# Kernel optimization log

Measured on AMD Instinct MI355X. Metric: run time of the kernel, lower is better.

## Reference

```python
import jax, jax.numpy as jnp
import numpy as np

B, TQ, TKV, D, H = 4, 1024, 2048, 1024, 16
DH = D // H


def setup_inputs() -> dict:
    key = jax.random.key(0)
    ks = jax.random.split(key, 12)
    s = 0.02
    return {
        "x": jax.random.normal(ks[0], (B, TQ, D), jnp.float32),
        "k_cache": jax.random.normal(ks[1], (B, TKV, D), jnp.float32),
        "v_cache": jax.random.normal(ks[2], (B, TKV, D), jnp.float32),
        "mask": jnp.zeros((TQ, TKV), jnp.float32),  # additive attention bias
        "Wq": jax.random.normal(ks[3], (D, D), jnp.float32) * s,
        "bq": jax.random.normal(ks[4], (D,), jnp.float32) * s,
        "Wk": jax.random.normal(ks[5], (D, D), jnp.float32) * s,  # key: no bias (Whisper-style)
        "Wv": jax.random.normal(ks[6], (D, D), jnp.float32) * s,
        "bv": jax.random.normal(ks[7], (D,), jnp.float32) * s,
        "Wo": jax.random.normal(ks[8], (D, D), jnp.float32) * s,
        "bo": jax.random.normal(ks[9], (D,), jnp.float32) * s,
    }


def reference(x, k_cache, v_cache, mask, Wq, bq, Wk, Wv, bv, Wo, bo):
    b, tq, d = x.shape
    scale = (d // H) ** -0.25
    # QKV projections (torch Linear: y = x @ W.T + b)
    q = x @ Wq.T + bq                      # [B,Tq,D]
    k_new = x @ Wk.T                       # [B,Tq,D] (key has no bias)
    v_new = x @ Wv.T + bv                  # [B,Tq,D]
    # KV-cache append: write last Tq positions
    k_cache = k_cache.at[:, -tq:, :].set(k_new)
    v_cache = v_cache.at[:, -tq:, :].set(v_new)
    # split heads
    qh = q.reshape(b, tq, H, DH) * scale           # [B,Tq,H,Dh]
    kh = k_cache.reshape(b, -1, H, DH) * scale     # [B,Tkv,H,Dh]
    vh = v_cache.reshape(b, -1, H, DH)             # [B,Tkv,H,Dh]
    qk = jnp.einsum("bqhd,bkhd->bhqk", qh, kh) + mask  # [B,H,Tq,Tkv]
    w = jax.nn.softmax(qk.astype(jnp.float32), axis=-1).astype(qh.dtype)
    wv = jnp.einsum("bhqk,bkhd->bqhd", w, vh).reshape(b, tq, d)
    out = wv @ Wo.T + bo
    return out, k_cache, v_cache
```

## Files before the change

### kernel.cpp

```cpp
#include <hip/hip_runtime.h>
#include <hip/hip_bf16.h>


typedef __bf16 bf16_t;
typedef __attribute__((ext_vector_type(4))) float f32x4;
typedef __attribute__((ext_vector_type(8))) __bf16 bf16x8;
typedef __attribute__((ext_vector_type(4))) __bf16 bf16x4;
typedef __attribute__((ext_vector_type(4))) unsigned short u16x4;

__device__ inline bf16x4 cvt4(float4 f) {
    bf16x4 o;
    o.x = (bf16_t)f.x; o.y = (bf16_t)f.y; o.z = (bf16_t)f.z; o.w = (bf16_t)f.w;
    return o;
}

__device__ inline void gload_lds16(const void* g, void* s) {
    __builtin_amdgcn_global_load_lds(
        (const __attribute__((address_space(1))) void*)g,
        (__attribute__((address_space(3))) void*)s, 16, 0, 0);
}

__device__ inline unsigned cvt_pk_bf16(float lo, float hi) {
    unsigned r;
    asm("v_cvt_pk_bf16_f32 %0, %1, %2" : "=v"(r) : "v"(lo), "v"(hi));
    return r;
}
__device__ inline void pswap32(unsigned& a, unsigned& b) {
    asm("v_permlane32_swap_b32 %0, %1" : "+v"(a), "+v"(b));
}
__device__ inline void pswap16(unsigned& a, unsigned& b) {
    asm("v_permlane16_swap_b32 %0, %1" : "+v"(a), "+v"(b));
}

#if __has_builtin(__builtin_amdgcn_exp2f)
__device__ inline float exp2_fast(float x) { return __builtin_amdgcn_exp2f(x); }
#else
__device__ inline float exp2_fast(float x) { return exp2f(x); }
#endif


__global__ void cast_f32_bf16_k(const float* __restrict__ src, bf16_t* __restrict__ dst, int n4) {
    int i = blockIdx.x * blockDim.x + threadIdx.x;
    if (i >= n4) return;
    float4 f = reinterpret_cast<const float4*>(src)[i];
    reinterpret_cast<bf16x4*>(dst)[i] = cvt4(f);
}

__global__ void build_wqkv_k(const float* __restrict__ Wq, const float* __restrict__ Wk,
                             const float* __restrict__ Wv, bf16_t* __restrict__ dst) {
    int i = blockIdx.x * blockDim.x + threadIdx.x;
    if (i >= 786432) return;
    int e0 = i * 4;
    int row = e0 >> 10;
    const float* src;
    if (row < 1024)       src = Wq + e0;
    else if (row < 2048)  src = Wk + (e0 - 1048576);
    else                  src = Wv + (e0 - 2097152);
    float4 f = *reinterpret_cast<const float4*>(src);
    reinterpret_cast<bf16x4*>(dst)[i] = cvt4(f);
}

__global__ void build_bias_k(const float* __restrict__ bq, const float* __restrict__ bv,
                             float* __restrict__ bias) {
    int i = blockIdx.x * blockDim.x + threadIdx.x;
    if (i >= 3072) return;
    float v;
    if (i < 1024)      v = bq[i];
    else if (i < 2048) v = 0.f;
    else               v = bv[i - 2048];
    bias[i] = v;
}

__global__ void copy_old2_k(const float* __restrict__ kc, const float* __restrict__ vc,
                            float* __restrict__ kout, float* __restrict__ vout,
                            bf16_t* __restrict__ k_bf) {
    int i = blockIdx.x * blockDim.x + threadIdx.x;
    if (i >= 2097152) return;
    int which = i >> 20;
    int ii = i & 1048575;
    int b = ii >> 18;
    int r = ii & 262143;
    size_t off = (size_t)b * 2097152 + (size_t)r * 4;
    if (which == 0) {
        float4 f = *reinterpret_cast<const float4*>(kc + off);
        *reinterpret_cast<float4*>(kout + off) = f;
        reinterpret_cast<bf16x4*>(k_bf + off)[0] = cvt4(f);
    } else {
        float4 f = *reinterpret_cast<const float4*>(vc + off);
        *reinterpret_cast<float4*>(vout + off) = f;
    }
}

__global__ __launch_bounds__(256) void transpose_v_k(const float* __restrict__ vout,
                                                     bf16_t* __restrict__ vT) {
    __shared__ bf16_t t[64][65];
    int blk = blockIdx.x;
    int kvt = blk >> 6;
    int bh  = blk & 63;
    int b = bh >> 4, h = bh & 15;
    int kv0 = kvt * 64;
    int tid = threadIdx.x;
    int c = tid & 63, r0 = tid >> 6;
    #pragma unroll
    for (int rr = r0; rr < 64; rr += 4)
        t[rr][c] = (bf16_t)vout[((size_t)b * 2048 + kv0 + rr) * 1024 + h * 64 + c];
    __syncthreads();
    #pragma unroll
    for (int dd = r0; dd < 64; dd += 4)
        vT[((size_t)bh * 64 + dd) * 2048 + kv0 + c] = t[c][dd];
}

__global__ void mask_bf16_k(const float* __restrict__ mask, bf16_t* __restrict__ maskB) {
    int i = blockIdx.x * blockDim.x + threadIdx.x;
    if (i >= 2097152) return;
    int r   = i & 3;
    int c16 = (i >> 2) & 15;
    int qd  = (i >> 6) & 3;
    int kb  = (i >> 8) & 127;
    int qb  = i >> 15;
    float v = mask[(size_t)(qb * 16 + c16) * 2048 + kb * 16 + qd * 4 + r] * 1.4426950408889634f;
    maskB[i] = (bf16_t)v;
}

#define LDF(bufp, row, off) (*reinterpret_cast<const bf16x8*>(&(bufp)[(row) * 64 + (off)]))

__global__ __launch_bounds__(512, 2) void gemm8_k(const bf16_t* __restrict__ A,
                                                  const bf16_t* __restrict__ Bw,
                                                  const float* __restrict__ bias,
                                                  bf16_t* __restrict__ q_bf,
                                                  float* __restrict__ kout,
                                                  bf16_t* __restrict__ k_bf,
                                                  float* __restrict__ vout) {
    const int K = 1024;
    __shared__ __align__(16) bf16_t As[2][16384];
    __shared__ __align__(16) bf16_t Bs[2][16384];
    int m0 = blockIdx.x * 256, n0 = blockIdx.y * 256;
    int tid = threadIdx.x;
    int lane = tid & 63, w = tid >> 6;
    int wrM = w >> 2, wrN = w & 3;
    int col16 = lane & 15, quad = lane >> 4;
    int cx = (quad ^ (col16 & 7)) * 8;

    int sr = tid >> 3;
    int scb = ((tid & 7) ^ (sr & 7)) * 8;
    const bf16_t* ga = A + (size_t)(m0 + sr) * K + scb;
    const bf16_t* gb = Bw + (size_t)(n0 + sr) * K + scb;
    int ldst = sr * 64 + (tid & 7) * 8;

    auto stageA = [&](int d, int kt) {
        size_t ko = (size_t)kt * 64;
        gload_lds16(ga + ko, &As[d][ldst]);
        gload_lds16(ga + 64 * (size_t)K + ko, &As[d][ldst + 4096]);
        gload_lds16(ga + 128 * (size_t)K + ko, &As[d][ldst + 8192]);
        gload_lds16(ga + 192 * (size_t)K + ko, &As[d][ldst + 12288]);
    };
    auto stageB = [&](int d, int kt) {
        size_t ko = (size_t)kt * 64;
        gload_lds16(gb + ko, &Bs[d][ldst]);
        gload_lds16(gb + 64 * (size_t)K + ko, &Bs[d][ldst + 4096]);
        gload_lds16(gb + 128 * (size_t)K + ko, &Bs[d][ldst + 8192]);
        gload_lds16(gb + 192 * (size_t)K + ko, &Bs[d][ldst + 12288]);
    };

    int arow = wrM * 128 + col16;
    int brow = wrN * 64 + col16;

    f32x4 zero = {0.f, 0.f, 0.f, 0.f};
    f32x4 acc[8][4];
    #pragma unroll
    for (int mi = 0; mi < 8; mi++)
        #pragma unroll
        for (int ni = 0; ni < 4; ni++) acc[mi][ni] = zero;

    stageA(0, 0);
    stageB(0, 0);
    stageA(1, 1);
    asm volatile("s_waitcnt vmcnt(4)" ::: "memory");
    __builtin_amdgcn_s_barrier();

    for (int kt = 0; kt < 16; kt++) {
        int d = kt & 1;
        const bf16_t* Ad = As[d];
        const bf16_t* Bd = Bs[d];
        bf16x8 a0[4][2], bb0[2][2];
        #pragma unroll
        for (int mi = 0; mi < 4; mi++) {
            a0[mi][0] = LDF(Ad, arow + mi * 16, cx);
            a0[mi][1] = LDF(Ad, arow + mi * 16, cx ^ 32);
        }
        #pragma unroll
        for (int ni = 0; ni < 2; ni++) {
            bb0[ni][0] = LDF(Bd, brow + ni * 16, cx);
            bb0[ni][1] = LDF(Bd, brow + ni * 16, cx ^ 32);
        }
        if (kt < 15) stageB(d ^ 1, kt + 1);
        __builtin_amdgcn_s_barrier();
        __builtin_amdgcn_s_setprio(1);
        #pragma unroll
        for (int mi = 0; mi < 4; mi++)
            #pragma unroll
            for (int ni = 0; ni < 2; ni++) {
                acc[mi][ni] = __builtin_amdgcn_mfma_f32_16x16x32_bf16(a0[mi][0], bb0[ni][0], acc[mi][ni], 0, 0, 0);
                acc[mi][ni] = __builtin_amdgcn_mfma_f32_16x16x32_bf16(a0[mi][1], bb0[ni][1], acc[mi][ni], 0, 0, 0);
            }
        __builtin_amdgcn_s_setprio(0);
        __builtin_amdgcn_s_barrier();
        bf16x8 bb1[2][2];
        #pragma unroll
        for (int ni = 0; ni < 2; ni++) {
            bb1[ni][0] = LDF(Bd, brow + 32 + ni * 16, cx);
            bb1[ni][1] = LDF(Bd, brow + 32 + ni * 16, cx ^ 32);
        }
        __builtin_amdgcn_s_barrier();
        __builtin_amdgcn_s_setprio(1);
        #pragma unroll
        for (int mi = 0; mi < 4; mi++)
            #pragma unroll
            for (int ni = 0; ni < 2; ni++) {
                acc[mi][ni + 2] = __builtin_amdgcn_mfma_f32_16x16x32_bf16(a0[mi][0], bb1[ni][0], acc[mi][ni + 2], 0, 0, 0);
                acc[mi][ni + 2] = __builtin_amdgcn_mfma_f32_16x16x32_bf16(a0[mi][1], bb1[ni][1], acc[mi][ni + 2], 0, 0, 0);
            }
        __builtin_amdgcn_s_setprio(0);
        __builtin_amdgcn_s_barrier();
        bf16x8 a1[4][2];
        #pragma unroll
        for (int mi = 0; mi < 4; mi++) {
            a1[mi][0] = LDF(Ad, arow + 64 + mi * 16, cx);
            a1[mi][1] = LDF(Ad, arow + 64 + mi * 16, cx ^ 32);
        }
        __builtin_amdgcn_s_barrier();
        __builtin_amdgcn_s_setprio(1);
        #pragma unroll
        for (int mi = 0; mi < 4; mi++)
            #pragma unroll
            for (int ni = 0; ni < 2; ni++) {
                acc[mi + 4][ni] = __builtin_amdgcn_mfma_f32_16x16x32_bf16(a1[mi][0], bb0[ni][0], acc[mi + 4][ni], 0, 0, 0);
                acc[mi + 4][ni] = __builtin_amdgcn_mfma_f32_16x16x32_bf16(a1[mi][1], bb0[ni][1], acc[mi + 4][ni], 0, 0, 0);
            }
        __builtin_amdgcn_s_setprio(0);
        __builtin_amdgcn_s_barrier();
        if (kt < 14) {
            stageA(d, kt + 2);
            asm volatile("s_waitcnt vmcnt(4)" ::: "memory");
        } else {
            asm volatile("s_waitcnt vmcnt(0)" ::: "memory");
        }
        __builtin_amdgcn_s_barrier();
        __builtin_amdgcn_s_setprio(1);
        #pragma unroll
        for (int mi = 0; mi < 4; mi++)
            #pragma unroll
            for (int ni = 0; ni < 2; ni++) {
                acc[mi + 4][ni + 2] = __builtin_amdgcn_mfma_f32_16x16x32_bf16(a1[mi][0], bb1[ni][0], acc[mi + 4][ni + 2], 0, 0, 0);
                acc[mi + 4][ni + 2] = __builtin_amdgcn_mfma_f32_16x16x32_bf16(a1[mi][1], bb1[ni][1], acc[mi + 4][ni + 2], 0, 0, 0);
            }
        __builtin_amdgcn_s_setprio(0);
        __builtin_amdgcn_s_barrier();
    }

    int mb = m0 + wrM * 128 + quad * 4;
    int nb = n0 + wrN * 64 + col16;
    if (n0 < 1024) {
        #pragma unroll
        for (int ni = 0; ni < 4; ni++) {
            int gn = nb + ni * 16;
            float bia = bias[gn];
            #pragma unroll
            for (int mi = 0; mi < 8; mi++) {
                int gm = mb + mi * 16;
                #pragma unroll
                for (int r = 0; r < 4; r++)
                    q_bf[(size_t)(gm + r) * 1024 + gn] = (bf16_t)(acc[mi][ni][r] + bia);
            }
        }
    } else if (n0 < 2048) {
        #pragma unroll
        for (int ni = 0; ni < 4; ni++) {
            int gn = nb + ni * 16;
            float bia = bias[gn];
            int n2 = gn - 1024;
            #pragma unroll
            for (int mi = 0; mi < 8; mi++) {
                int gm = mb + mi * 16;
                #pragma unroll
                for (int r = 0; r < 4; r++) {
                    int gmr = gm + r;
                    int b = gmr >> 10, t = gmr & 1023;
                    size_t off = ((size_t)b * 2048 + 1024 + t) * 1024 + n2;
                    float v = acc[mi][ni][r] + bia;
                    kout[off] = v;
                    k_bf[off] = (bf16_t)v;
                }
            }
        }
    } else {
        #pragma unroll
        for (int ni = 0; ni < 4; ni++) {
            int gn = nb + ni * 16;
            float bia = bias[gn];
            int n2 = gn - 2048;
            #pragma unroll
            for (int mi = 0; mi < 8; mi++) {
                int gm = mb + mi * 16;
                #pragma unroll
                for (int r = 0; r < 4; r++) {
                    int gmr = gm + r;
                    int b = gmr >> 10, t = gmr & 1023;
                    vout[((size_t)b * 2048 + 1024 + t) * 1024 + n2] = acc[mi][ni][r] + bia;
                }
            }
        }
    }
}

__global__ __launch_bounds__(256) void gemm_wo_k(const bf16_t* __restrict__ A,
                                                 const bf16_t* __restrict__ Bw,
                                                 const float* __restrict__ bias,
                                                 float* __restrict__ out0) {
    const int K = 1024;
    __shared__ __align__(16) bf16_t As[2][4096];
    __shared__ __align__(16) bf16_t Bs[2][4096];
    int m0 = blockIdx.x * 128, n0 = blockIdx.y * 128;
    int tid = threadIdx.x;
    int lane = tid & 63, w = tid >> 6;
    int wr = w >> 1, wc = w & 1;
    int col16 = lane & 15, quad = lane >> 4;

    int srow = tid >> 2;
    int scol = ((tid & 3) ^ ((srow >> 1) & 3)) * 8;
    const bf16_t* ga = A + (size_t)(m0 + srow) * K + scol;
    const bf16_t* gb = Bw + (size_t)(n0 + srow) * K + scol;

    int qsw = (quad ^ ((col16 >> 1) & 3)) * 8;

    f32x4 zero = {0.f, 0.f, 0.f, 0.f};
    f32x4 acc[4][4];
    #pragma unroll
    for (int mi = 0; mi < 4; mi++)
        #pragma unroll
        for (int ni = 0; ni < 4; ni++) acc[mi][ni] = zero;

    auto stageg = [&](int d, int k) {
        gload_lds16(ga + k, &As[d][tid * 8]);
        gload_lds16(ga + (size_t)64 * K + k, &As[d][tid * 8 + 2048]);
        gload_lds16(gb + k, &Bs[d][tid * 8]);
        gload_lds16(gb + (size_t)64 * K + k, &Bs[d][tid * 8 + 2048]);
    };

    stageg(0, 0);
    __syncthreads();
    for (int kb = 0; kb < 32; kb++) {
        int cur = kb & 1;
        if (kb < 31) stageg(cur ^ 1, (kb + 1) * 32);
        bf16x8 af[4], bfr[4];
        #pragma unroll
        for (int mi = 0; mi < 4; mi++)
            af[mi] = *reinterpret_cast<const bf16x8*>(
                &As[cur][(wr * 64 + mi * 16 + col16) * 32 + qsw]);
        #pragma unroll
        for (int ni = 0; ni < 4; ni++)
            bfr[ni] = *reinterpret_cast<const bf16x8*>(
                &Bs[cur][(wc * 64 + ni * 16 + col16) * 32 + qsw]);
        #pragma unroll
        for (int mi = 0; mi < 4; mi++)
            #pragma unroll
            for (int ni = 0; ni < 4; ni++)
                acc[mi][ni] = __builtin_amdgcn_mfma_f32_16x16x32_bf16(
                    af[mi], bfr[ni], acc[mi][ni], 0, 0, 0);
        __syncthreads();
    }

    int mbase = m0 + wr * 64 + quad * 4;
    int nbase = n0 + wc * 64 + col16;
    #pragma unroll
    for (int ni = 0; ni < 4; ni++) {
        int gn = nbase + ni * 16;
        float bia = bias[gn];
        #pragma unroll
        for (int mi = 0; mi < 4; mi++) {
            int gm = mbase + mi * 16;
            #pragma unroll
            for (int r = 0; r < 4; r++)
                out0[(size_t)(gm + r) * 1024 + gn] = acc[mi][ni][r] + bia;
        }
    }
}

__global__ __launch_bounds__(512, 4) void attn_k(const bf16_t* __restrict__ qbf,
                                                 const bf16_t* __restrict__ kbf,
                                                 const bf16_t* __restrict__ vT,
                                                 const bf16_t* __restrict__ maskB,
                                                 bf16_t* __restrict__ wv) {
    __shared__ __align__(16) bf16_t Ks[2][4096];
    __shared__ __align__(16) bf16_t Vs[2][4096];
    int logical = (blockIdx.x & 7) * 64 + (blockIdx.x >> 3);
    int bh = logical >> 3;
    int qtb = logical & 7;
    int b = bh >> 4, h = bh & 15;
    int tid = threadIdx.x, w = tid >> 6, lane = tid & 63;
    int col16 = lane & 15, quad = lane >> 4;
    int c7 = col16 & 7;
    int cx = (quad ^ c7) * 8;
    int qr0 = qtb * 128 + w * 16;

    int sr = tid >> 3, sc = (tid & 7) ^ ((tid >> 3) & 7);
    const bf16_t* kg = kbf + ((size_t)b * 2048 + sr) * 1024 + h * 64 + sc * 8;
    const bf16_t* vg = vT + ((size_t)bh * 64 + sr) * 2048 + sc * 8;
    auto stage = [&](int d, int kv0) {
        gload_lds16(kg + (size_t)kv0 * 1024, &Ks[d][tid * 8]);
        gload_lds16(vg + kv0, &Vs[d][tid * 8]);
    };

    const bf16_t* qrow = qbf + ((size_t)b * 1024 + qr0 + col16) * 1024 + h * 64;
    bf16x8 aq0 = *reinterpret_cast<const bf16x8*>(qrow + quad * 8);
    bf16x8 aq1 = *reinterpret_cast<const bf16x8*>(qrow + 32 + quad * 8);

    const bf16_t* mbase = maskB + (size_t)(qtb * 8 + w) * 32768 + quad * 64 + col16 * 4;

    f32x4 zero = {0.f, 0.f, 0.f, 0.f};
    f32x4 oacc[4];
    #pragma unroll
    for (int dt = 0; dt < 4; dt++) oacc[dt] = zero;
    float lrow = 0.f;

    stage(0, 0);
    __syncthreads();

    for (int t = 0; t < 32; t++) {
        int cur = t & 1;
        if (t < 31) stage(cur ^ 1, (t + 1) * 64);
        unsigned pk[4][2];
        #pragma unroll
        for (int nt = 0; nt < 4; nt++) {
            const bf16_t* kr = &Ks[cur][(nt * 16 + col16) * 64];
            bf16x8 k0 = *reinterpret_cast<const bf16x8*>(kr + cx);
            bf16x8 k1 = *reinterpret_cast<const bf16x8*>(kr + (cx ^ 32));
            f32x4 s = __builtin_amdgcn_mfma_f32_16x16x32_bf16(k0, aq0, zero, 0, 0, 0);
            s = __builtin_amdgcn_mfma_f32_16x16x32_bf16(k1, aq1, s, 0, 0, 0);
            u16x4 m4 = *reinterpret_cast<const u16x4*>(mbase + (size_t)(t * 4 + nt) * 256);
            float p[4];
            #pragma unroll
            for (int r = 0; r < 4; r++) {
                float mv = __builtin_bit_cast(float, (unsigned)m4[r] << 16);
                p[r] = exp2_fast(fmaf(s[r], 0.18033688011112042f, mv));
                lrow += p[r];
            }
            pk[nt][0] = cvt_pk_bf16(p[0], p[1]);
            pk[nt][1] = cvt_pk_bf16(p[2], p[3]);
        }
        union PB { unsigned u[4]; bf16x8 v; };
        PB pf0, pf1;
        {
            unsigned a0 = pk[0][0], b0 = pk[1][0];
            pswap32(a0, b0); pswap16(a0, b0);
            pf0.u[0] = a0; pf0.u[2] = b0;
            unsigned a1 = pk[0][1], b1 = pk[1][1];
            pswap32(a1, b1); pswap16(a1, b1);
            pf0.u[1] = a1; pf0.u[3] = b1;
            unsigned a2 = pk[2][0], b2 = pk[3][0];
            pswap32(a2, b2); pswap16(a2, b2);
            pf1.u[0] = a2; pf1.u[2] = b2;
            unsigned a3 = pk[2][1], b3 = pk[3][1];
            pswap32(a3, b3); pswap16(a3, b3);
            pf1.u[1] = a3; pf1.u[3] = b3;
        }
        #pragma unroll
        for (int dt = 0; dt < 4; dt++) {
            const bf16_t* vr = &Vs[cur][(dt * 16 + col16) * 64];
            bf16x8 v0 = *reinterpret_cast<const bf16x8*>(vr + cx);
            bf16x8 v1 = *reinterpret_cast<const bf16x8*>(vr + (cx ^ 32));
            oacc[dt] = __builtin_amdgcn_mfma_f32_16x16x32_bf16(v0, pf0.v, oacc[dt], 0, 0, 0);
            oacc[dt] = __builtin_amdgcn_mfma_f32_16x16x32_bf16(v1, pf1.v, oacc[dt], 0, 0, 0);
        }
        __syncthreads();
    }

    lrow += __shfl_xor(lrow, 16);
    lrow += __shfl_xor(lrow, 32);
    float inv = 1.f / lrow;
    bf16_t* orow = wv + ((size_t)b * 1024 + qr0 + col16) * 1024 + h * 64 + quad * 4;
    #pragma unroll
    for (int dt = 0; dt < 4; dt++) {
        bf16x4 o4;
        #pragma unroll
        for (int r = 0; r < 4; r++) o4[r] = (bf16_t)(oacc[dt][r] * inv);
        *reinterpret_cast<bf16x4*>(orow + dt * 16) = o4;
    }
}


extern "C" void kernel_launch(void* const* d_in, const int* in_sizes, int n_in,
                              void* d_out, int out_size, void* d_ws, size_t ws_size,
                              hipStream_t stream) {
    const float* x    = (const float*)d_in[0];
    const float* kc   = (const float*)d_in[1];
    const float* vc   = (const float*)d_in[2];
    const float* mask = (const float*)d_in[3];
    const float* Wq   = (const float*)d_in[4];
    const float* bq   = (const float*)d_in[5];
    const float* Wk   = (const float*)d_in[6];
    const float* Wv   = (const float*)d_in[7];
    const float* bv   = (const float*)d_in[8];
    const float* Wo   = (const float*)d_in[9];
    const float* bo   = (const float*)d_in[10];

    float* out0 = (float*)d_out;
    float* kout = out0 + 4194304;
    float* vout = out0 + 12582912;

    char* ws = (char*)d_ws;
    bf16_t* x_bf     = (bf16_t*)(ws);
    bf16_t* wqkv_bf  = (bf16_t*)(ws + 8388608);
    bf16_t* wo_bf    = (bf16_t*)(ws + 14680064);
    float*  bias_qkv = (float*)(ws + 16777216);
    bf16_t* q_bf     = (bf16_t*)(ws + 16789504);
    bf16_t* k_bf     = (bf16_t*)(ws + 25178112);
    bf16_t* vT_bf    = (bf16_t*)(ws + 41955328);
    bf16_t* wv_bf    = (bf16_t*)(ws + 58732544);
    bf16_t* maskB    = (bf16_t*)(ws + 67108864);

    cast_f32_bf16_k<<<4096, 256, 0, stream>>>(x, x_bf, 1048576);
    build_wqkv_k<<<3072, 256, 0, stream>>>(Wq, Wk, Wv, wqkv_bf);
    cast_f32_bf16_k<<<1024, 256, 0, stream>>>(Wo, wo_bf, 262144);
    build_bias_k<<<12, 256, 0, stream>>>(bq, bv, bias_qkv);
    mask_bf16_k<<<8192, 256, 0, stream>>>(mask, maskB);
    copy_old2_k<<<8192, 256, 0, stream>>>(kc, vc, kout, vout, k_bf);
    gemm8_k<<<dim3(16, 12), 512, 0, stream>>>(x_bf, wqkv_bf, bias_qkv,
                                              q_bf, kout, k_bf, vout);
    transpose_v_k<<<2048, 256, 0, stream>>>(vout, vT_bf);
    attn_k<<<512, 512, 0, stream>>>(q_bf, k_bf, vT_bf, maskB, wv_bf);
    gemm_wo_k<<<dim3(32, 8), 256, 0, stream>>>(wv_bf, wo_bf, bo, out0);
}
```

Measured before the change: 316.2 us.

## Use inline-asm LDS reads with explicit waits and remap GEMM block order

Replaces compiler-generated LDS vector loads with inline ds_read_b128 plus explicit lgkmcnt(0) waits and sched barriers in the QKV GEMM, output GEMM and attention kernels. This pins the load/MFMA ordering the code expects. It also permutes the QKV GEMM block index so neighbouring blocks share operand tiles in cache. The attention kernel now waits per tile for its loads, which may serialise LDS latency that the compiler previously hid.

```diff
diff --git a/kernel.cpp b/kernel.cpp
--- a/kernel.cpp
+++ b/kernel.cpp
@@ -19,6 +19,17 @@
         (const __attribute__((address_space(1))) void*)g,
         (__attribute__((address_space(3))) void*)s, 16, 0, 0);
 }
+
+__device__ inline bf16x8 ldsr128(const bf16_t* p) {
+    bf16x8 d;
+    unsigned a = (unsigned)(size_t)(const __attribute__((address_space(3))) bf16_t*)p;
+    asm volatile("ds_read_b128 %0, %1" : "=v"(d) : "v"(a));
+    return d;
+}
+
+#define WAIT_LGKM0 do { asm volatile("s_waitcnt lgkmcnt(0)" ::: "memory"); \
+                        __builtin_amdgcn_sched_barrier(0); } while (0)
+#define WAIT_VM(n) asm volatile("s_waitcnt vmcnt(" #n ")" ::: "memory")
 
 __device__ inline unsigned cvt_pk_bf16(float lo, float hi) {
     unsigned r;
@@ -122,8 +133,6 @@
     maskB[i] = (bf16_t)v;
 }
 
-#define LDF(bufp, row, off) (*reinterpret_cast<const bf16x8*>(&(bufp)[(row) * 64 + (off)]))
-
 __global__ __launch_bounds__(512, 2) void gemm8_k(const bf16_t* __restrict__ A,
                                                   const bf16_t* __restrict__ Bw,
                                                   const float* __restrict__ bias,
@@ -134,7 +143,9 @@
     const int K = 1024;
     __shared__ __align__(16) bf16_t As[2][16384];
     __shared__ __align__(16) bf16_t Bs[2][16384];
-    int m0 = blockIdx.x * 256, n0 = blockIdx.y * 256;
+    int flat = blockIdx.y * 16 + blockIdx.x;
+    int logi = (flat & 7) * 24 + (flat >> 3);
+    int m0 = (logi / 12) * 256, n0 = (logi % 12) * 256;
     int tid = threadIdx.x;
     int lane = tid & 63, w = tid >> 6;
     int wrM = w >> 2, wrN = w & 3;
@@ -175,7 +186,7 @@
     stageA(0, 0);
     stageB(0, 0);
     stageA(1, 1);
-    asm volatile("s_waitcnt vmcnt(4)" ::: "memory");
+    WAIT_VM(4);
     __builtin_amdgcn_s_barrier();
 
     for (int kt = 0; kt < 16; kt++) {
@@ -185,16 +196,19 @@
         bf16x8 a0[4][2], bb0[2][2];
         #pragma unroll
         for (int mi = 0; mi < 4; mi++) {
-            a0[mi][0] = LDF(Ad, arow + mi * 16, cx);
-            a0[mi][1] = LDF(Ad, arow + mi * 16, cx ^ 32);
+            const bf16_t* p = &Ad[(arow + mi * 16) * 64];
+            a0[mi][0] = ldsr128(p + cx);
+            a0[mi][1] = ldsr128(p + (cx ^ 32));
         }
         #pragma unroll
         for (int ni = 0; ni < 2; ni++) {
-            bb0[ni][0] = LDF(Bd, brow + ni * 16, cx);
-            bb0[ni][1] = LDF(Bd, brow + ni * 16, cx ^ 32);
+            const bf16_t* p = &Bd[(brow + ni * 16) * 64];
+            bb0[ni][0] = ldsr128(p + cx);
+            bb0[ni][1] = ldsr128(p + (cx ^ 32));
         }
         if (kt < 15) stageB(d ^ 1, kt + 1);
         __builtin_amdgcn_s_barrier();
+        WAIT_LGKM0;
         __builtin_amdgcn_s_setprio(1);
         #pragma unroll
         for (int mi = 0; mi < 4; mi++)
@@ -208,10 +222,12 @@
         bf16x8 bb1[2][2];
         #pragma unroll
         for (int ni = 0; ni < 2; ni++) {
-            bb1[ni][0] = LDF(Bd, brow + 32 + ni * 16, cx);
-            bb1[ni][1] = LDF(Bd, brow + 32 + ni * 16, cx ^ 32);
-        }
-        __builtin_amdgcn_s_barrier();
+            const bf16_t* p = &Bd[(brow + 32 + ni * 16) * 64];
+            bb1[ni][0] = ldsr128(p + cx);
+            bb1[ni][1] = ldsr128(p + (cx ^ 32));
+        }
+        __builtin_amdgcn_s_barrier();
+        WAIT_LGKM0;
         __builtin_amdgcn_s_setprio(1);
         #pragma unroll
         for (int mi = 0; mi < 4; mi++)
@@ -225,10 +241,12 @@
         bf16x8 a1[4][2];
         #pragma unroll
         for (int mi = 0; mi < 4; mi++) {
-            a1[mi][0] = LDF(Ad, arow + 64 + mi * 16, cx);
-            a1[mi][1] = LDF(Ad, arow + 64 + mi * 16, cx ^ 32);
-        }
-        __builtin_amdgcn_s_barrier();
+            const bf16_t* p = &Ad[(arow + 64 + mi * 16) * 64];
+            a1[mi][0] = ldsr128(p + cx);
+            a1[mi][1] = ldsr128(p + (cx ^ 32));
+        }
+        __builtin_amdgcn_s_barrier();
+        WAIT_LGKM0;
         __builtin_amdgcn_s_setprio(1);
         #pragma unroll
         for (int mi = 0; mi < 4; mi++)
@@ -241,9 +259,9 @@
         __builtin_amdgcn_s_barrier();
         if (kt < 14) {
             stageA(d, kt + 2);
-            asm volatile("s_waitcnt vmcnt(4)" ::: "memory");
+            WAIT_VM(4);
         } else {
-            asm volatile("s_waitcnt vmcnt(0)" ::: "memory");
+            WAIT_VM(0);
         }
         __builtin_amdgcn_s_barrier();
         __builtin_amdgcn_s_setprio(1);
@@ -355,12 +373,11 @@
         bf16x8 af[4], bfr[4];
         #pragma unroll
         for (int mi = 0; mi < 4; mi++)
-            af[mi] = *reinterpret_cast<const bf16x8*>(
-                &As[cur][(wr * 64 + mi * 16 + col16) * 32 + qsw]);
+            af[mi] = ldsr128(&As[cur][(wr * 64 + mi * 16 + col16) * 32 + qsw]);
         #pragma unroll
         for (int ni = 0; ni < 4; ni++)
-            bfr[ni] = *reinterpret_cast<const bf16x8*>(
-                &Bs[cur][(wc * 64 + ni * 16 + col16) * 32 + qsw]);
+            bfr[ni] = ldsr128(&Bs[cur][(wc * 64 + ni * 16 + col16) * 32 + qsw]);
+        WAIT_LGKM0;
         #pragma unroll
         for (int mi = 0; mi < 4; mi++)
             #pragma unroll
@@ -433,8 +450,9 @@
         #pragma unroll
         for (int nt = 0; nt < 4; nt++) {
             const bf16_t* kr = &Ks[cur][(nt * 16 + col16) * 64];
-            bf16x8 k0 = *reinterpret_cast<const bf16x8*>(kr + cx);
-            bf16x8 k1 = *reinterpret_cast<const bf16x8*>(kr + (cx ^ 32));
+            bf16x8 k0 = ldsr128(kr + cx);
+            bf16x8 k1 = ldsr128(kr + (cx ^ 32));
+            WAIT_LGKM0;
             f32x4 s = __builtin_amdgcn_mfma_f32_16x16x32_bf16(k0, aq0, zero, 0, 0, 0);
             s = __builtin_amdgcn_mfma_f32_16x16x32_bf16(k1, aq1, s, 0, 0, 0);
             u16x4 m4 = *reinterpret_cast<const u16x4*>(mbase + (size_t)(t * 4 + nt) * 256);
@@ -467,8 +485,9 @@
         #pragma unroll
         for (int dt = 0; dt < 4; dt++) {
             const bf16_t* vr = &Vs[cur][(dt * 16 + col16) * 64];
-            bf16x8 v0 = *reinterpret_cast<const bf16x8*>(vr + cx);
-            bf16x8 v1 = *reinterpret_cast<const bf16x8*>(vr + (cx ^ 32));
+            bf16x8 v0 = ldsr128(vr + cx);
+            bf16x8 v1 = ldsr128(vr + (cx ^ 32));
+            WAIT_LGKM0;
             oacc[dt] = __builtin_amdgcn_mfma_f32_16x16x32_bf16(v0, pf0.v, oacc[dt], 0, 0, 0);
             oacc[dt] = __builtin_amdgcn_mfma_f32_16x16x32_bf16(v1, pf1.v, oacc[dt], 0, 0, 0);
         }
```

After: 319.6 us. No clear change (+1.1%).
